# Performance work log

Hardware: AMD Instinct MI355X
Metric: run time of the kernel (lower is better)

The kernel has to match this reference:

```python
import jax, jax.numpy as jnp
import numpy as np

B, N, K = 4, 4096, 16
D_POINTS, D_MODEL = 64, 128


def setup_inputs() -> dict:
    key = jax.random.key(0)
    ks = jax.random.split(key, 18)
    rn = lambda k, shp, s=0.05: (jax.random.normal(k, shp, jnp.float32) * s)
    return {
        "xyz": jax.random.normal(ks[0], (B, N, 3), jnp.float32),
        "features": jax.random.normal(ks[1], (B, N, D_POINTS), jnp.float32),
        # fc_delta: Linear(3,d_model) -> ReLU -> Linear(d_model,d_model)
        "Wd1": rn(ks[2], (3, D_MODEL)), "bd1": rn(ks[3], (D_MODEL,)),
        "Wd2": rn(ks[4], (D_MODEL, D_MODEL)), "bd2": rn(ks[5], (D_MODEL,)),
        # fc1: Linear(d_points, d_model)
        "Wf1": rn(ks[6], (D_POINTS, D_MODEL)), "bf1": rn(ks[7], (D_MODEL,)),
        # w_qs / w_ks / w_vs: Linear(d_model, d_model, bias=False)
        "Wq": rn(ks[8], (D_MODEL, D_MODEL)),
        "Wk": rn(ks[9], (D_MODEL, D_MODEL)),
        "Wv": rn(ks[10], (D_MODEL, D_MODEL)),
        # fc_gamma: Linear(d_model,d_model) -> ReLU -> Linear(d_model,d_model)
        "Wg1": rn(ks[11], (D_MODEL, D_MODEL)), "bg1": rn(ks[12], (D_MODEL,)),
        "Wg2": rn(ks[13], (D_MODEL, D_MODEL)), "bg2": rn(ks[14], (D_MODEL,)),
        # fc2: Linear(d_model, d_points)
        "Wo": rn(ks[15], (D_MODEL, D_POINTS)), "bo": rn(ks[16], (D_POINTS,)),
    }


def reference(xyz, features, Wd1, bd1, Wd2, bd2, Wf1, bf1, Wq, Wk, Wv,
              Wg1, bg1, Wg2, bg2, Wo, bo):
    sq = jnp.sum(xyz * xyz, axis=-1)
    d2 = sq[:, :, None] + sq[:, None, :] - 2.0 * jnp.einsum('bnd,bmd->bnm', xyz, xyz)
    # argsort()[:, :, :k] == k smallest distances (self included)
    _, knn_idx = jax.lax.top_k(-d2, K)  # [B,N,K] int32

    gather = jax.vmap(lambda a, i: a[i])  # per-batch fancy gather along point axis
    knn_xyz = gather(xyz, knn_idx)                       # [B,N,K,3]
    rel = xyz[:, :, None, :] - knn_xyz                   # [B,N,K,3]
    pos_enc = jax.nn.relu(rel @ Wd1 + bd1) @ Wd2 + bd2   # [B,N,K,D]

    shortcut = features
    f = features @ Wf1 + bf1                             # [B,N,D]
    knn_f = gather(f, knn_idx)                           # [B,N,K,D]

    q = f @ Wq                                           # [B,N,D]
    k = knn_f @ Wk                                       # [B,N,K,D]
    v = knn_f @ Wv                                       # [B,N,K,D]

    attn = q[:, :, None, :] - k + pos_enc                # [B,N,K,D]
    attn = jax.nn.relu(attn @ Wg1 + bg1) @ Wg2 + bg2
    attn = jax.nn.softmax(attn / np.sqrt(D_MODEL).astype(np.float32), axis=-2)

    res = jnp.einsum('bnkf,bnkf->bnf', attn, v + pos_enc)  # [B,N,D]
    return res @ Wo + bo + shortcut                        # [B,N,d_points]
```

## Files before the change

kernel.cpp:

```cpp
#include <hip/hip_runtime.h>
#include <hip/hip_bf16.h>

#define NPTS 4096
#define BATCH 4
#define BN (BATCH * NPTS)
#define DMODEL 128
#define DPTS 64
#define KNBR 16
#define SWS 136

typedef unsigned short u16;
typedef unsigned int u32;
typedef unsigned long long u64;
typedef short bh8 __attribute__((ext_vector_type(8)));
typedef float f32x4 __attribute__((ext_vector_type(4)));

__device__ __forceinline__ float bfu(u16 u) {
    union { u32 i; float f; } c; c.i = ((u32)u) << 16; return c.f;
}
__device__ __forceinline__ u16 f2u(float x) {
    u32 u = __float_as_uint(x);
    u32 r = u + 0x7FFFu + ((u >> 16) & 1u);
    return (u16)(r >> 16);
}
__device__ __forceinline__ u32 pack2(float a, float b) {
    return (u32)f2u(a) | ((u32)f2u(b) << 16);
}
__device__ __forceinline__ float ldr(const void* p, long i, int mode) {
    return mode == 0 ? bfu(((const u16*)p)[i]) : ((const float*)p)[i];
}
__device__ __forceinline__ void str(void* p, long i, float v, int mode) {
    if (mode == 0) ((u16*)p)[i] = f2u(v);
    else ((float*)p)[i] = v;
}
__device__ __forceinline__ int detect_mode(const void* Wq) {
    const u16* w = (const u16*)Wq;
    int lane = threadIdx.x & 63;
    int tot = 0;
#pragma unroll
    for (int r = 0; r < 4; ++r) {
        unsigned e = (w[lane + r * 64] >> 7) & 0xFFu;
        bool wild = (e >= 132u) || (e > 0u && e <= 90u);
        tot += (int)__popcll(__ballot(wild));
    }
    return tot > 32 ? 1 : 0;
}

__global__ __launch_bounds__(256) void prep_kernel(
    const void* __restrict__ Wd2, const void* __restrict__ Wg1, const void* __restrict__ Wg2,
    const void* __restrict__ Wo, const void* __restrict__ Wq, const void* __restrict__ Wk,
    const void* __restrict__ Wv, const void* __restrict__ Wf1, const void* __restrict__ xyz,
    u16* __restrict__ WdT2, u16* __restrict__ WgT1, u16* __restrict__ WgT2,
    u16* __restrict__ WoT, u16* __restrict__ WqT, u16* __restrict__ WkT,
    u16* __restrict__ WvT, u16* __restrict__ WfT, uint2* __restrict__ cloud) {
    int mode = detect_mode(Wq);
    int gid = blockIdx.x * 256 + threadIdx.x;
    if (gid < 6 * 16384) {
        int m = gid >> 14, o = gid & 16383;
        int n = o >> 7, i = o & 127;
        const void* W = (m == 0) ? Wd2 : (m == 1) ? Wg1 : (m == 2) ? Wg2
                      : (m == 3) ? Wq  : (m == 4) ? Wk  : Wv;
        u16* D = (m == 0) ? WdT2 : (m == 1) ? WgT1 : (m == 2) ? WgT2
               : (m == 3) ? WqT  : (m == 4) ? WkT  : WvT;
        D[o] = f2u(ldr(W, (long)i * 128 + n, mode));
    } else if (gid < 6 * 16384 + 8192) {
        int o = gid - 6 * 16384;
        int n = o >> 6, k2 = o & 63;
        WfT[o] = f2u(ldr(Wf1, (long)k2 * 128 + n, mode));
    } else if (gid < 6 * 16384 + 16384) {
        int o2 = gid - 6 * 16384 - 8192;
        int col = o2 >> 7, i = o2 & 127;
        WoT[o2] = f2u(ldr(Wo, (long)i * 64 + col, mode));
    } else if (gid < 6 * 16384 + 16384 + 16384) {
        int i = gid - (6 * 16384 + 16384);
        float gx = ldr(xyz, (long)i * 3 + 0, mode);
        float gy = ldr(xyz, (long)i * 3 + 1, mode);
        float gz = ldr(xyz, (long)i * 3 + 2, mode);
        uint2 pk;
        pk.x = (u32)f2u(gx) | ((u32)f2u(gy) << 16);
        pk.y = (u32)f2u(gz);
        cloud[i] = pk;
    }
}

__global__ __launch_bounds__(256) void qkv_kernel(
    const void* __restrict__ feat, const void* __restrict__ bf1v, const void* __restrict__ WqRaw,
    const u16* __restrict__ WfT, const u16* __restrict__ WqT,
    const u16* __restrict__ WkT, const u16* __restrict__ WvT,
    u16* __restrict__ qw, u16* __restrict__ kfw, u16* __restrict__ vfw) {
    int mode = detect_mode(WqRaw);
    __shared__ __align__(16) u16 sFeat[64 * 72];
    __shared__ __align__(16) u16 sF[64 * SWS];
    const int t = threadIdx.x;
    const int p0 = blockIdx.x * 64;
    const int lane = t & 63, w = t >> 6;
    const int rg = (w & 1) * 32, cg = (w >> 1) * 64;
    const int lm = lane & 15, lq = lane >> 4;

    for (int i = t; i < 512; i += 256) {
        int r = i >> 3, c8 = i & 7;
        u16 tmp[8];
        if (mode == 0) {
            *(uint4*)tmp = *((const uint4*)feat + (long)(p0 + r) * 8 + c8);
        } else {
            const float* fp = (const float*)feat + (long)(p0 + r) * 64 + c8 * 8;
#pragma unroll
            for (int u = 0; u < 8; ++u) tmp[u] = f2u(fp[u]);
        }
        *(uint4*)(sFeat + r * 72 + c8 * 8) = *(uint4*)tmp;
    }
    __syncthreads();

    {
        f32x4 acc[2][4];
#pragma unroll
        for (int rt = 0; rt < 2; ++rt)
#pragma unroll
            for (int ct = 0; ct < 4; ++ct) { acc[rt][ct][0]=0.f; acc[rt][ct][1]=0.f; acc[rt][ct][2]=0.f; acc[rt][ct][3]=0.f; }
#pragma unroll
        for (int kk = 0; kk < 2; ++kk) {
            const int ko = kk * 32 + lq * 8;
            bh8 a0 = *(const bh8*)(sFeat + (rg + lm) * 72 + ko);
            bh8 a1 = *(const bh8*)(sFeat + (rg + 16 + lm) * 72 + ko);
            bh8 bq[4];
#pragma unroll
            for (int ct = 0; ct < 4; ++ct)
                bq[ct] = *(const bh8*)(WfT + (long)(cg + ct * 16 + lm) * 64 + ko);
#pragma unroll
            for (int ct = 0; ct < 4; ++ct) {
                acc[0][ct] = __builtin_amdgcn_mfma_f32_16x16x32_bf16(a0, bq[ct], acc[0][ct], 0, 0, 0);
                acc[1][ct] = __builtin_amdgcn_mfma_f32_16x16x32_bf16(a1, bq[ct], acc[1][ct], 0, 0, 0);
            }
        }
#pragma unroll
        for (int rt = 0; rt < 2; ++rt)
#pragma unroll
            for (int ct = 0; ct < 4; ++ct) {
                const int col = cg + ct * 16 + lm;
                const float bj = ldr(bf1v, col, mode);
#pragma unroll
                for (int r4 = 0; r4 < 4; ++r4) {
                    int row = rg + rt * 16 + lq * 4 + r4;
                    u32 u = (u32)f2u(acc[rt][ct][r4] + bj);
                    u32 o = __shfl_xor(u, 1);
                    if ((lane & 1) == 0)
                        *(u32*)(sF + row * SWS + col) = u | (o << 16);
                }
            }
    }
    __syncthreads();

    {
        const int m = blockIdx.y;
        const u16* Wm = (m == 0) ? WqT : (m == 1) ? WkT : WvT;
        u16* Om = (m == 0) ? qw : (m == 1) ? kfw : vfw;
        f32x4 acc[2][4];
#pragma unroll
        for (int rt = 0; rt < 2; ++rt)
#pragma unroll
            for (int ct = 0; ct < 4; ++ct) { acc[rt][ct][0]=0.f; acc[rt][ct][1]=0.f; acc[rt][ct][2]=0.f; acc[rt][ct][3]=0.f; }
#pragma unroll
        for (int kk = 0; kk < 4; ++kk) {
            const int ko = kk * 32 + lq * 8;
            bh8 a0 = *(const bh8*)(sF + (rg + lm) * SWS + ko);
            bh8 a1 = *(const bh8*)(sF + (rg + 16 + lm) * SWS + ko);
            bh8 bq[4];
#pragma unroll
            for (int ct = 0; ct < 4; ++ct)
                bq[ct] = *(const bh8*)(Wm + (long)(cg + ct * 16 + lm) * 128 + ko);
#pragma unroll
            for (int ct = 0; ct < 4; ++ct) {
                acc[0][ct] = __builtin_amdgcn_mfma_f32_16x16x32_bf16(a0, bq[ct], acc[0][ct], 0, 0, 0);
                acc[1][ct] = __builtin_amdgcn_mfma_f32_16x16x32_bf16(a1, bq[ct], acc[1][ct], 0, 0, 0);
            }
        }
#pragma unroll
        for (int rt = 0; rt < 2; ++rt)
#pragma unroll
            for (int ct = 0; ct < 4; ++ct) {
                const int col = cg + ct * 16 + lm;
#pragma unroll
                for (int r4 = 0; r4 < 4; ++r4) {
                    int row = rg + rt * 16 + lq * 4 + r4;
                    u32 u = (u32)f2u(acc[rt][ct][r4]);
                    u32 o = __shfl_xor(u, 1);
                    if ((lane & 1) == 0)
                        *(u32*)(Om + (long)(p0 + row) * DMODEL + col) = u | (o << 16);
                }
            }
    }
}

__global__ __launch_bounds__(256) void knn_kernel(
    const uint2* __restrict__ cloud, int* __restrict__ knnIdx) {
    const int t = threadIdx.x, lane = t & 63, w = t >> 6;
    const int p0 = blockIdx.x * 4;
    const long bbase = (long)(p0 >> 12) * NPTS;
    const uint2* cl = cloud + bbase;

    const int pl = (p0 & (NPTS - 1)) + w;
    uint2 qv = cl[pl];
    const float px = __uint_as_float(qv.x << 16);
    const float py = __uint_as_float(qv.x & 0xFFFF0000u);
    const float pz = __uint_as_float(qv.y << 16);

    u64 kv;
    {
        uint2 c = cl[lane];
        float cx = __uint_as_float(c.x << 16);
        float cy = __uint_as_float(c.x & 0xFFFF0000u);
        float cz = __uint_as_float(c.y << 16);
        float key = fmaf(px * cx + py * cy + pz * cz, -2.f,
                         cx * cx + cy * cy + cz * cz);
        u32 uk = __float_as_uint(key);
        uk ^= (u32)((int)uk >> 31) | 0x80000000u;
        kv = ((u64)uk << 32) | (u32)lane;
#pragma unroll
        for (int k = 2; k <= 64; k <<= 1) {
#pragma unroll
            for (int j = k >> 1; j > 0; j >>= 1) {
                u64 other = __shfl_xor(kv, j);
                bool keepMin = ((lane & j) == 0) == ((lane & k) == 0);
                bool smaller = kv < other;
                kv = (keepMin == smaller) ? kv : other;
            }
        }
    }
    u32 Tu = __builtin_amdgcn_readlane((u32)(kv >> 32), 15);

    uint2 cd0 = cl[64 + lane];
    uint2 cd1 = cl[128 + lane];
#pragma unroll 1
    for (int it = 0; it < 32; ++it) {
        const int base = 64 + it * 128;
        uint2 c0 = cd0, c1 = cd1;
        if (it < 31) {
            int n0 = base + 128 + lane;
            int n1 = n0 + 64 > 4095 ? 4095 : n0 + 64;
            cd0 = cl[n0];
            cd1 = cl[n1];
        }
        float cx0 = __uint_as_float(c0.x << 16);
        float cy0 = __uint_as_float(c0.x & 0xFFFF0000u);
        float cz0 = __uint_as_float(c0.y << 16);
        float cx1 = __uint_as_float(c1.x << 16);
        float cy1 = __uint_as_float(c1.x & 0xFFFF0000u);
        float cz1 = __uint_as_float(c1.y << 16);
        float k0 = fmaf(px * cx0 + py * cy0 + pz * cz0, -2.f,
                        cx0 * cx0 + cy0 * cy0 + cz0 * cz0);
        float k1 = fmaf(px * cx1 + py * cy1 + pz * cz1, -2.f,
                        cx1 * cx1 + cy1 * cy1 + cz1 * cz1);
        u32 u0 = __float_as_uint(k0); u0 ^= (u32)((int)u0 >> 31) | 0x80000000u;
        u32 u1 = __float_as_uint(k1); u1 ^= (u32)((int)u1 >> 31) | 0x80000000u;
        if (it == 31) u1 = 0xFFFFFFFFu;
        u32 umin = (u0 < u1) ? u0 : u1;
        unsigned long long mask = __ballot(umin < Tu);
        while (mask) {
            int l = __ffsll(mask) - 1;
            mask &= mask - 1;
            u32 a0 = __builtin_amdgcn_readlane(u0, l);
            u32 a1 = __builtin_amdgcn_readlane(u1, l);
            if (a0 < Tu) {
                u64 cand = ((u64)a0 << 32) | (u32)(base + l);
                u64 prev = __shfl_up(kv, 1);
                if (lane == 0) prev = 0;
                kv = (prev > cand) ? prev : ((kv > cand) ? cand : kv);
                Tu = __builtin_amdgcn_readlane((u32)(kv >> 32), 15);
            }
            if (a1 < Tu) {
                u64 cand = ((u64)a1 << 32) | (u32)(base + 64 + l);
                u64 prev = __shfl_up(kv, 1);
                if (lane == 0) prev = 0;
                kv = (prev > cand) ? prev : ((kv > cand) ? cand : kv);
                Tu = __builtin_amdgcn_readlane((u32)(kv >> 32), 15);
            }
        }
    }
    if (lane < 16) knnIdx[(long)(p0 + w) * 16 + lane] = (int)(u32)kv;
}

#define ATT_SA 0
#define ATT_SREL 17408
#define ATT_SBIAS 18432
#define ATT_SQ 19968
#define SMEM_BYTES 20992

__global__ __launch_bounds__(256, 4) void fused_kernel(
    const uint2* __restrict__ cloud, const int* __restrict__ knnIdx,
    const void* __restrict__ feat,
    const void* __restrict__ Wd1, const void* __restrict__ bd1, const void* __restrict__ bd2,
    const void* __restrict__ bg1, const void* __restrict__ bg2, const void* __restrict__ bo,
    const void* __restrict__ WqRaw,
    const u16* __restrict__ WdT2, const u16* __restrict__ WgT1, const u16* __restrict__ WgT2,
    const u16* __restrict__ WoT,
    const u16* __restrict__ qw, const u16* __restrict__ kfw, const u16* __restrict__ vfw,
    void* __restrict__ out) {
    int mode = detect_mode(WqRaw);
    __shared__ __align__(16) char smem[SMEM_BYTES];
    __shared__ int sIdx[64];
    u16* sA   = (u16*)(smem + ATT_SA);
    float (*sRel)[4] = (float(*)[4])(smem + ATT_SREL);
    float* sBias = (float*)(smem + ATT_SBIAS);
    u16* sQ   = (u16*)(smem + ATT_SQ);

    const int t = threadIdx.x, lane = t & 63, w = t >> 6;
    const int lm = lane & 15, lq = lane >> 4;
    const int rg = (w & 1) * 32, cg = (w >> 1) * 64;
    const int p0 = blockIdx.x * 4;
    const long bbase = (long)(p0 >> 12) * NPTS;
    const uint2* cl = cloud + bbase;

    for (int i = t; i < 384; i += 256) {
        const void* b = (i < 128) ? bd2 : (i < 256) ? bg1 : bg2;
        sBias[i] = ldr(b, i & 127, mode);
    }
    ((u32*)sQ)[t] = ((const u32*)(qw + (long)p0 * DMODEL))[t];
    const int ch = 2 * lane;
    const float wd0a = ldr(Wd1, ch, mode),       wd0b = ldr(Wd1, ch + 1, mode);
    const float wd1a = ldr(Wd1, 128 + ch, mode), wd1b = ldr(Wd1, 128 + ch + 1, mode);
    const float wd2a = ldr(Wd1, 256 + ch, mode), wd2b = ldr(Wd1, 256 + ch + 1, mode);
    const float bd1a = ldr(bd1, ch, mode),       bd1b = ldr(bd1, ch + 1, mode);
    if (t < 64) {
        int idx = knnIdx[(long)p0 * 16 + t];
        sIdx[t] = idx;
        int pl2 = (p0 & (NPTS - 1)) + (t >> 4);
        uint2 pv = cl[pl2];
        uint2 nv = cl[idx];
        sRel[t][0] = __uint_as_float(pv.x << 16)          - __uint_as_float(nv.x << 16);
        sRel[t][1] = __uint_as_float(pv.x & 0xFFFF0000u)  - __uint_as_float(nv.x & 0xFFFF0000u);
        sRel[t][2] = __uint_as_float(pv.y << 16)          - __uint_as_float(nv.y << 16);
    }
    __syncthreads();

#pragma unroll
    for (int i = 0; i < 16; ++i) {
        int r = w * 16 + i;
        float4 rl = *(const float4*)sRel[r];
        float h0 = fmaxf(bd1a + rl.x * wd0a + rl.y * wd1a + rl.z * wd2a, 0.f);
        float h1 = fmaxf(bd1b + rl.x * wd0b + rl.y * wd1b + rl.z * wd2b, 0.f);
        *(u32*)(sA + r * SWS + ch) = pack2(h0, h1);
    }
    __syncthreads();

    u32 pe[2][4][2];
    {
        f32x4 acc[2][4];
#pragma unroll
        for (int rt = 0; rt < 2; ++rt)
#pragma unroll
            for (int ct = 0; ct < 4; ++ct) { acc[rt][ct][0]=0.f; acc[rt][ct][1]=0.f; acc[rt][ct][2]=0.f; acc[rt][ct][3]=0.f; }
#pragma unroll
        for (int kk = 0; kk < 4; ++kk) {
            const int ko = kk * 32 + lq * 8;
            bh8 a0 = *(const bh8*)(sA + (rg + lm) * SWS + ko);
            bh8 a1 = *(const bh8*)(sA + (rg + 16 + lm) * SWS + ko);
            bh8 bq[4];
#pragma unroll
            for (int ct = 0; ct < 4; ++ct)
                bq[ct] = *(const bh8*)(WdT2 + (long)(cg + ct * 16 + lm) * 128 + ko);
#pragma unroll
            for (int ct = 0; ct < 4; ++ct) {
                acc[0][ct] = __builtin_amdgcn_mfma_f32_16x16x32_bf16(a0, bq[ct], acc[0][ct], 0, 0, 0);
                acc[1][ct] = __builtin_amdgcn_mfma_f32_16x16x32_bf16(a1, bq[ct], acc[1][ct], 0, 0, 0);
            }
        }
#pragma unroll
        for (int rt = 0; rt < 2; ++rt)
#pragma unroll
            for (int ct = 0; ct < 4; ++ct) {
                const float bj = sBias[cg + ct * 16 + lm];
                pe[rt][ct][0] = pack2(acc[rt][ct][0] + bj, acc[rt][ct][1] + bj);
                pe[rt][ct][1] = pack2(acc[rt][ct][2] + bj, acc[rt][ct][3] + bj);
            }
    }
    __syncthreads();

#pragma unroll
    for (int rt = 0; rt < 2; ++rt) {
        const int pt = (w & 1) * 2 + rt;
        int id4[4];
#pragma unroll
        for (int r4 = 0; r4 < 4; ++r4)
            id4[r4] = sIdx[rg + rt * 16 + lq * 4 + r4];
#pragma unroll
        for (int ct = 0; ct < 4; ++ct) {
            const int col = cg + ct * 16 + lm;
            const float qv = bfu(sQ[pt * DMODEL + col]);
#pragma unroll
            for (int r4 = 0; r4 < 4; ++r4) {
                const int row = rg + rt * 16 + lq * 4 + r4;
                u16 kfv = kfw[(bbase + id4[r4]) * (long)DMODEL + col];
                float pev = bfu((u16)(pe[rt][ct][r4 >> 1] >> (16 * (r4 & 1))));
                float a = qv - bfu(kfv) + pev;
                u32 u = (u32)f2u(a);
                u32 o = __shfl_xor(u, 1);
                if ((lm & 1) == 0)
                    *(u32*)(sA + row * SWS + col) = u | (o << 16);
            }
        }
    }
    __syncthreads();

    {
        f32x4 acc[2][4];
#pragma unroll
        for (int rt = 0; rt < 2; ++rt)
#pragma unroll
            for (int ct = 0; ct < 4; ++ct) { acc[rt][ct][0]=0.f; acc[rt][ct][1]=0.f; acc[rt][ct][2]=0.f; acc[rt][ct][3]=0.f; }
#pragma unroll
        for (int kk = 0; kk < 4; ++kk) {
            const int ko = kk * 32 + lq * 8;
            bh8 a0 = *(const bh8*)(sA + (rg + lm) * SWS + ko);
            bh8 a1 = *(const bh8*)(sA + (rg + 16 + lm) * SWS + ko);
            bh8 bq[4];
#pragma unroll
            for (int ct = 0; ct < 4; ++ct)
                bq[ct] = *(const bh8*)(WgT1 + (long)(cg + ct * 16 + lm) * 128 + ko);
#pragma unroll
            for (int ct = 0; ct < 4; ++ct) {
                acc[0][ct] = __builtin_amdgcn_mfma_f32_16x16x32_bf16(a0, bq[ct], acc[0][ct], 0, 0, 0);
                acc[1][ct] = __builtin_amdgcn_mfma_f32_16x16x32_bf16(a1, bq[ct], acc[1][ct], 0, 0, 0);
            }
        }
        __syncthreads();
#pragma unroll
        for (int rt = 0; rt < 2; ++rt)
#pragma unroll
            for (int ct = 0; ct < 4; ++ct) {
                const int col = cg + ct * 16 + lm;
                const float bj = sBias[128 + col];
#pragma unroll
                for (int r4 = 0; r4 < 4; ++r4) {
                    int row = rg + rt * 16 + lq * 4 + r4;
                    float v = fmaxf(acc[rt][ct][r4] + bj, 0.f);
                    u32 u = (u32)f2u(v);
                    u32 o = __shfl_xor(u, 1);
                    if ((lane & 1) == 0)
                        *(u32*)(sA + row * SWS + col) = u | (o << 16);
                }
            }
    }
    __syncthreads();

    {
        f32x4 acc[2][4];
#pragma unroll
        for (int rt = 0; rt < 2; ++rt)
#pragma unroll
            for (int ct = 0; ct < 4; ++ct) { acc[rt][ct][0]=0.f; acc[rt][ct][1]=0.f; acc[rt][ct][2]=0.f; acc[rt][ct][3]=0.f; }
#pragma unroll
        for (int kk = 0; kk < 4; ++kk) {
            const int ko = kk * 32 + lq * 8;
            bh8 a0 = *(const bh8*)(sA + (rg + lm) * SWS + ko);
            bh8 a1 = *(const bh8*)(sA + (rg + 16 + lm) * SWS + ko);
            bh8 bq[4];
#pragma unroll
            for (int ct = 0; ct < 4; ++ct)
                bq[ct] = *(const bh8*)(WgT2 + (long)(cg + ct * 16 + lm) * 128 + ko);
#pragma unroll
            for (int ct = 0; ct < 4; ++ct) {
                acc[0][ct] = __builtin_amdgcn_mfma_f32_16x16x32_bf16(a0, bq[ct], acc[0][ct], 0, 0, 0);
                acc[1][ct] = __builtin_amdgcn_mfma_f32_16x16x32_bf16(a1, bq[ct], acc[1][ct], 0, 0, 0);
            }
        }
        __syncthreads();

        const float inv = 0.08838834764831845f;
#pragma unroll
        for (int rt = 0; rt < 2; ++rt) {
            const int pt = (w & 1) * 2 + rt;
            int id4[4];
#pragma unroll
            for (int r4 = 0; r4 < 4; ++r4)
                id4[r4] = sIdx[rg + rt * 16 + lq * 4 + r4];
#pragma unroll
            for (int ct = 0; ct < 4; ++ct) {
                const int col = cg + ct * 16 + lm;
                const float bj = sBias[256 + col];
                float l0 = acc[rt][ct][0] + bj;
                float l1 = acc[rt][ct][1] + bj;
                float l2 = acc[rt][ct][2] + bj;
                float l3 = acc[rt][ct][3] + bj;
                float m = fmaxf(fmaxf(l0, l1), fmaxf(l2, l3));
                m = fmaxf(m, __shfl_xor(m, 16));
                m = fmaxf(m, __shfl_xor(m, 32));
                float s = 0.f, r = 0.f;
#pragma unroll
                for (int r4 = 0; r4 < 4; ++r4) {
                    float l = (r4 == 0) ? l0 : (r4 == 1) ? l1 : (r4 == 2) ? l2 : l3;
                    u16 vv = vfw[(bbase + id4[r4]) * (long)DMODEL + col];
                    float pev = bfu((u16)(pe[rt][ct][r4 >> 1] >> (16 * (r4 & 1))));
                    float e = __expf((l - m) * inv);
                    s += e;
                    r += e * (bfu(vv) + pev);
                }
                s += __shfl_xor(s, 16); s += __shfl_xor(s, 32);
                r += __shfl_xor(r, 16); r += __shfl_xor(r, 32);
                u32 u = (u32)f2u(r / s);
                u32 o = __shfl_xor(u, 1);
                if (lq == 0 && (lm & 1) == 0)
                    *(u32*)(sA + pt * SWS + col) = u | (o << 16);
            }
        }
    }
    __syncthreads();

    {
        const int col = w * 16 + lm;
        f32x4 acc = {0.f, 0.f, 0.f, 0.f};
#pragma unroll
        for (int kk = 0; kk < 4; ++kk) {
            const int ko = kk * 32 + lq * 8;
            bh8 aa = *(const bh8*)(sA + lm * SWS + ko);
            bh8 bb = *(const bh8*)(WoT + (long)col * DMODEL + ko);
            acc = __builtin_amdgcn_mfma_f32_16x16x32_bf16(aa, bb, acc, 0, 0, 0);
        }
        if (lq == 0) {
            float bov = ldr(bo, col, mode);
#pragma unroll
            for (int r4 = 0; r4 < 4; ++r4) {
                long p = p0 + r4;
                float v = acc[r4] + bov + ldr(feat, p * DPTS + col, mode);
                str(out, p * DPTS + col, v, mode);
            }
        }
    }
}

extern "C" void kernel_launch(void* const* d_in, const int* in_sizes, int n_in,
                              void* d_out, int out_size, void* d_ws, size_t ws_size,
                              hipStream_t stream) {
    (void)in_sizes; (void)n_in; (void)out_size; (void)ws_size;
    char* ws = (char*)d_ws;
    u16* qw   = (u16*)(ws + 256);
    u16* kfw  = qw + (long)BN * DMODEL;
    u16* vfw  = kfw + (long)BN * DMODEL;
    u16* WdT2 = vfw + (long)BN * DMODEL;
    u16* WgT1 = WdT2 + 16384;
    u16* WgT2 = WgT1 + 16384;
    u16* WoT  = WgT2 + 16384;
    u16* WqT  = WoT + 8192;
    u16* WkT  = WqT + 16384;
    u16* WvT  = WkT + 16384;
    u16* WfT  = WvT + 16384;
    uint2* cloud = (uint2*)(WfT + 8192);
    int* knnIdx = (int*)(cloud + BN);

    prep_kernel<<<512, 256, 0, stream>>>(d_in[4], d_in[11], d_in[13], d_in[15],
                                         d_in[8], d_in[9], d_in[10], d_in[6], d_in[0],
                                         WdT2, WgT1, WgT2, WoT, WqT, WkT, WvT, WfT,
                                         cloud);
    qkv_kernel<<<dim3(BN / 64, 3), 256, 0, stream>>>(d_in[1], d_in[7], d_in[8],
                                                     WfT, WqT, WkT, WvT, qw, kfw, vfw);
    knn_kernel<<<BN / 4, 256, 0, stream>>>(cloud, knnIdx);
    fused_kernel<<<BN / 4, 256, 0, stream>>>(cloud, knnIdx, d_in[1],
                                             d_in[2], d_in[3], d_in[5],
                                             d_in[12], d_in[14], d_in[16], d_in[8],
                                             WdT2, WgT1, WgT2, WoT,
                                             qw, kfw, vfw, d_out);
}
```

Measured before the change: 321.5 us.

## Double fused kernel to 512 threads and prefetch gathered K/V features early

The fused attention kernel moves from 256 to 512 threads per block. Each of the 8 waves now owns one point (16 neighbor rows) and a 64-column slice instead of two points, which halves per-wave accumulator registers. The gathers of neighbor key and value features are issued early into packed registers so their global latency overlaps with the positional-encoding and gamma MLP work. The trade-off is more threads per block, so occupancy now depends on the new launch bounds, and the final output projection leaves half the waves idle.

```diff
diff --git a/kernel.cpp b/kernel.cpp
--- a/kernel.cpp
+++ b/kernel.cpp
@@ -285,7 +285,7 @@
 #define ATT_SQ 19968
 #define SMEM_BYTES 20992
 
-__global__ __launch_bounds__(256, 4) void fused_kernel(
+__global__ __launch_bounds__(512, 6) void fused_kernel(
     const uint2* __restrict__ cloud, const int* __restrict__ knnIdx,
     const void* __restrict__ feat,
     const void* __restrict__ Wd1, const void* __restrict__ bd1, const void* __restrict__ bd2,
@@ -305,16 +305,17 @@
 
     const int t = threadIdx.x, lane = t & 63, w = t >> 6;
     const int lm = lane & 15, lq = lane >> 4;
-    const int rg = (w & 1) * 32, cg = (w >> 1) * 64;
+    const int pt = w & 3;
+    const int rg = pt * 16, cg = (w >> 2) * 64;
     const int p0 = blockIdx.x * 4;
     const long bbase = (long)(p0 >> 12) * NPTS;
     const uint2* cl = cloud + bbase;
 
-    for (int i = t; i < 384; i += 256) {
+    for (int i = t; i < 384; i += 512) {
         const void* b = (i < 128) ? bd2 : (i < 256) ? bg1 : bg2;
         sBias[i] = ldr(b, i & 127, mode);
     }
-    ((u32*)sQ)[t] = ((const u32*)(qw + (long)p0 * DMODEL))[t];
+    if (t < 256) ((u32*)sQ)[t] = ((const u32*)(qw + (long)p0 * DMODEL))[t];
     const int ch = 2 * lane;
     const float wd0a = ldr(Wd1, ch, mode),       wd0b = ldr(Wd1, ch + 1, mode);
     const float wd1a = ldr(Wd1, 128 + ch, mode), wd1b = ldr(Wd1, 128 + ch + 1, mode);
@@ -332,9 +333,25 @@
     }
     __syncthreads();
 
-#pragma unroll
-    for (int i = 0; i < 16; ++i) {
-        int r = w * 16 + i;
+    int id4[4];
+#pragma unroll
+    for (int r4 = 0; r4 < 4; ++r4)
+        id4[r4] = sIdx[rg + lq * 4 + r4];
+    u32 kfp[4][2];
+#pragma unroll
+    for (int ct = 0; ct < 4; ++ct) {
+        const int col = cg + ct * 16 + lm;
+        u16 a = kfw[(bbase + id4[0]) * (long)DMODEL + col];
+        u16 b = kfw[(bbase + id4[1]) * (long)DMODEL + col];
+        u16 c = kfw[(bbase + id4[2]) * (long)DMODEL + col];
+        u16 d = kfw[(bbase + id4[3]) * (long)DMODEL + col];
+        kfp[ct][0] = (u32)a | ((u32)b << 16);
+        kfp[ct][1] = (u32)c | ((u32)d << 16);
+    }
+
+#pragma unroll
+    for (int i = 0; i < 8; ++i) {
+        int r = w * 8 + i;
         float4 rl = *(const float4*)sRel[r];
         float h0 = fmaxf(bd1a + rl.x * wd0a + rl.y * wd1a + rl.z * wd2a, 0.f);
         float h1 = fmaxf(bd1b + rl.x * wd0b + rl.y * wd1b + rl.z * wd2b, 0.f);
@@ -342,57 +359,84 @@
     }
     __syncthreads();
 
-    u32 pe[2][4][2];
+    u32 pe[4][2];
     {
-        f32x4 acc[2][4];
-#pragma unroll
-        for (int rt = 0; rt < 2; ++rt)
-#pragma unroll
-            for (int ct = 0; ct < 4; ++ct) { acc[rt][ct][0]=0.f; acc[rt][ct][1]=0.f; acc[rt][ct][2]=0.f; acc[rt][ct][3]=0.f; }
+        f32x4 acc[4];
+#pragma unroll
+        for (int ct = 0; ct < 4; ++ct) { acc[ct][0]=0.f; acc[ct][1]=0.f; acc[ct][2]=0.f; acc[ct][3]=0.f; }
 #pragma unroll
         for (int kk = 0; kk < 4; ++kk) {
             const int ko = kk * 32 + lq * 8;
             bh8 a0 = *(const bh8*)(sA + (rg + lm) * SWS + ko);
-            bh8 a1 = *(const bh8*)(sA + (rg + 16 + lm) * SWS + ko);
-            bh8 bq[4];
-#pragma unroll
-            for (int ct = 0; ct < 4; ++ct)
-                bq[ct] = *(const bh8*)(WdT2 + (long)(cg + ct * 16 + lm) * 128 + ko);
-#pragma unroll
-            for (int ct = 0; ct < 4; ++ct) {
-                acc[0][ct] = __builtin_amdgcn_mfma_f32_16x16x32_bf16(a0, bq[ct], acc[0][ct], 0, 0, 0);
-                acc[1][ct] = __builtin_amdgcn_mfma_f32_16x16x32_bf16(a1, bq[ct], acc[1][ct], 0, 0, 0);
-            }
-        }
-#pragma unroll
-        for (int rt = 0; rt < 2; ++rt)
-#pragma unroll
-            for (int ct = 0; ct < 4; ++ct) {
-                const float bj = sBias[cg + ct * 16 + lm];
-                pe[rt][ct][0] = pack2(acc[rt][ct][0] + bj, acc[rt][ct][1] + bj);
-                pe[rt][ct][1] = pack2(acc[rt][ct][2] + bj, acc[rt][ct][3] + bj);
-            }
-    }
-    __syncthreads();
-
-#pragma unroll
-    for (int rt = 0; rt < 2; ++rt) {
-        const int pt = (w & 1) * 2 + rt;
-        int id4[4];
-#pragma unroll
-        for (int r4 = 0; r4 < 4; ++r4)
-            id4[r4] = sIdx[rg + rt * 16 + lq * 4 + r4];
+#pragma unroll
+            for (int ct = 0; ct < 4; ++ct) {
+                bh8 bq = *(const bh8*)(WdT2 + (long)(cg + ct * 16 + lm) * 128 + ko);
+                acc[ct] = __builtin_amdgcn_mfma_f32_16x16x32_bf16(a0, bq, acc[ct], 0, 0, 0);
+            }
+        }
+#pragma unroll
+        for (int ct = 0; ct < 4; ++ct) {
+            const float bj = sBias[cg + ct * 16 + lm];
+            pe[ct][0] = pack2(acc[ct][0] + bj, acc[ct][1] + bj);
+            pe[ct][1] = pack2(acc[ct][2] + bj, acc[ct][3] + bj);
+        }
+    }
+    __syncthreads();
+
+#pragma unroll
+    for (int ct = 0; ct < 4; ++ct) {
+        const int col = cg + ct * 16 + lm;
+        const float qv = bfu(sQ[pt * DMODEL + col]);
+#pragma unroll
+        for (int r4 = 0; r4 < 4; ++r4) {
+            const int row = rg + lq * 4 + r4;
+            float kfv = bfu((u16)(kfp[ct][r4 >> 1] >> (16 * (r4 & 1))));
+            float pev = bfu((u16)(pe[ct][r4 >> 1] >> (16 * (r4 & 1))));
+            float a = qv - kfv + pev;
+            u32 u = (u32)f2u(a);
+            u32 o = __shfl_xor(u, 1);
+            if ((lm & 1) == 0)
+                *(u32*)(sA + row * SWS + col) = u | (o << 16);
+        }
+    }
+    __syncthreads();
+
+    u32 vvp[4][2];
+#pragma unroll
+    for (int ct = 0; ct < 4; ++ct) {
+        const int col = cg + ct * 16 + lm;
+        u16 a = vfw[(bbase + id4[0]) * (long)DMODEL + col];
+        u16 b = vfw[(bbase + id4[1]) * (long)DMODEL + col];
+        u16 c = vfw[(bbase + id4[2]) * (long)DMODEL + col];
+        u16 d = vfw[(bbase + id4[3]) * (long)DMODEL + col];
+        vvp[ct][0] = (u32)a | ((u32)b << 16);
+        vvp[ct][1] = (u32)c | ((u32)d << 16);
+    }
+
+    {
+        f32x4 acc[4];
+#pragma unroll
+        for (int ct = 0; ct < 4; ++ct) { acc[ct][0]=0.f; acc[ct][1]=0.f; acc[ct][2]=0.f; acc[ct][3]=0.f; }
+#pragma unroll
+        for (int kk = 0; kk < 4; ++kk) {
+            const int ko = kk * 32 + lq * 8;
+            bh8 a0 = *(const bh8*)(sA + (rg + lm) * SWS + ko);
+#pragma unroll
+            for (int ct = 0; ct < 4; ++ct) {
+                bh8 bq = *(const bh8*)(WgT1 + (long)(cg + ct * 16 + lm) * 128 + ko);
+                acc[ct] = __builtin_amdgcn_mfma_f32_16x16x32_bf16(a0, bq, acc[ct], 0, 0, 0);
+            }
+        }
+        __syncthreads();
 #pragma unroll
         for (int ct = 0; ct < 4; ++ct) {
             const int col = cg + ct * 16 + lm;
-            const float qv = bfu(sQ[pt * DMODEL + col]);
+            const float bj = sBias[128 + col];
 #pragma unroll
             for (int r4 = 0; r4 < 4; ++r4) {
-                const int row = rg + rt * 16 + lq * 4 + r4;
-                u16 kfv = kfw[(bbase + id4[r4]) * (long)DMODEL + col];
-                float pev = bfu((u16)(pe[rt][ct][r4 >> 1] >> (16 * (r4 & 1))));
-                float a = qv - bfu(kfv) + pev;
-                u32 u = (u32)f2u(a);
+                int row = rg + lq * 4 + r4;
+                float v = fmaxf(acc[ct][r4] + bj, 0.f);
+                u32 u = (u32)f2u(v);
                 u32 o = __shfl_xor(u, 1);
                 if ((lm & 1) == 0)
                     *(u32*)(sA + row * SWS + col) = u | (o << 16);
@@ -402,110 +446,54 @@
     __syncthreads();
 
     {
-        f32x4 acc[2][4];
-#pragma unroll
-        for (int rt = 0; rt < 2; ++rt)
-#pragma unroll
-            for (int ct = 0; ct < 4; ++ct) { acc[rt][ct][0]=0.f; acc[rt][ct][1]=0.f; acc[rt][ct][2]=0.f; acc[rt][ct][3]=0.f; }
+        f32x4 acc[4];
+#pragma unroll
+        for (int ct = 0; ct < 4; ++ct) { acc[ct][0]=0.f; acc[ct][1]=0.f; acc[ct][2]=0.f; acc[ct][3]=0.f; }
 #pragma unroll
         for (int kk = 0; kk < 4; ++kk) {
             const int ko = kk * 32 + lq * 8;
             bh8 a0 = *(const bh8*)(sA + (rg + lm) * SWS + ko);
-            bh8 a1 = *(const bh8*)(sA + (rg + 16 + lm) * SWS + ko);
-            bh8 bq[4];
-#pragma unroll
-            for (int ct = 0; ct < 4; ++ct)
-                bq[ct] = *(const bh8*)(WgT1 + (long)(cg + ct * 16 + lm) * 128 + ko);
-#pragma unroll
-            for (int ct = 0; ct < 4; ++ct) {
-                acc[0][ct] = __builtin_amdgcn_mfma_f32_16x16x32_bf16(a0, bq[ct], acc[0][ct], 0, 0, 0);
-                acc[1][ct] = __builtin_amdgcn_mfma_f32_16x16x32_bf16(a1, bq[ct], acc[1][ct], 0, 0, 0);
+#pragma unroll
+            for (int ct = 0; ct < 4; ++ct) {
+                bh8 bq = *(const bh8*)(WgT2 + (long)(cg + ct * 16 + lm) * 128 + ko);
+                acc[ct] = __builtin_amdgcn_mfma_f32_16x16x32_bf16(a0, bq, acc[ct], 0, 0, 0);
             }
         }
         __syncthreads();
-#pragma unroll
-        for (int rt = 0; rt < 2; ++rt)
-#pragma unroll
-            for (int ct = 0; ct < 4; ++ct) {
-                const int col = cg + ct * 16 + lm;
-                const float bj = sBias[128 + col];
-#pragma unroll
-                for (int r4 = 0; r4 < 4; ++r4) {
-                    int row = rg + rt * 16 + lq * 4 + r4;
-                    float v = fmaxf(acc[rt][ct][r4] + bj, 0.f);
-                    u32 u = (u32)f2u(v);
-                    u32 o = __shfl_xor(u, 1);
-                    if ((lane & 1) == 0)
-                        *(u32*)(sA + row * SWS + col) = u | (o << 16);
-                }
-            }
-    }
-    __syncthreads();
-
-    {
-        f32x4 acc[2][4];
-#pragma unroll
-        for (int rt = 0; rt < 2; ++rt)
-#pragma unroll
-            for (int ct = 0; ct < 4; ++ct) { acc[rt][ct][0]=0.f; acc[rt][ct][1]=0.f; acc[rt][ct][2]=0.f; acc[rt][ct][3]=0.f; }
-#pragma unroll
-        for (int kk = 0; kk < 4; ++kk) {
-            const int ko = kk * 32 + lq * 8;
-            bh8 a0 = *(const bh8*)(sA + (rg + lm) * SWS + ko);
-            bh8 a1 = *(const bh8*)(sA + (rg + 16 + lm) * SWS + ko);
-            bh8 bq[4];
-#pragma unroll
-            for (int ct = 0; ct < 4; ++ct)
-                bq[ct] = *(const bh8*)(WgT2 + (long)(cg + ct * 16 + lm) * 128 + ko);
-#pragma unroll
-            for (int ct = 0; ct < 4; ++ct) {
-                acc[0][ct] = __builtin_amdgcn_mfma_f32_16x16x32_bf16(a0, bq[ct], acc[0][ct], 0, 0, 0);
-                acc[1][ct] = __builtin_amdgcn_mfma_f32_16x16x32_bf16(a1, bq[ct], acc[1][ct], 0, 0, 0);
-            }
-        }
-        __syncthreads();
 
         const float inv = 0.08838834764831845f;
 #pragma unroll
-        for (int rt = 0; rt < 2; ++rt) {
-            const int pt = (w & 1) * 2 + rt;
-            int id4[4];
-#pragma unroll
-            for (int r4 = 0; r4 < 4; ++r4)
-                id4[r4] = sIdx[rg + rt * 16 + lq * 4 + r4];
-#pragma unroll
-            for (int ct = 0; ct < 4; ++ct) {
-                const int col = cg + ct * 16 + lm;
-                const float bj = sBias[256 + col];
-                float l0 = acc[rt][ct][0] + bj;
-                float l1 = acc[rt][ct][1] + bj;
-                float l2 = acc[rt][ct][2] + bj;
-                float l3 = acc[rt][ct][3] + bj;
-                float m = fmaxf(fmaxf(l0, l1), fmaxf(l2, l3));
-                m = fmaxf(m, __shfl_xor(m, 16));
-                m = fmaxf(m, __shfl_xor(m, 32));
-                float s = 0.f, r = 0.f;
-#pragma unroll
-                for (int r4 = 0; r4 < 4; ++r4) {
-                    float l = (r4 == 0) ? l0 : (r4 == 1) ? l1 : (r4 == 2) ? l2 : l3;
-                    u16 vv = vfw[(bbase + id4[r4]) * (long)DMODEL + col];
-                    float pev = bfu((u16)(pe[rt][ct][r4 >> 1] >> (16 * (r4 & 1))));
-                    float e = __expf((l - m) * inv);
-                    s += e;
-                    r += e * (bfu(vv) + pev);
-                }
-                s += __shfl_xor(s, 16); s += __shfl_xor(s, 32);
-                r += __shfl_xor(r, 16); r += __shfl_xor(r, 32);
-                u32 u = (u32)f2u(r / s);
-                u32 o = __shfl_xor(u, 1);
-                if (lq == 0 && (lm & 1) == 0)
-                    *(u32*)(sA + pt * SWS + col) = u | (o << 16);
-            }
-        }
-    }
-    __syncthreads();
-
-    {
+        for (int ct = 0; ct < 4; ++ct) {
+            const int col = cg + ct * 16 + lm;
+            const float bj = sBias[256 + col];
+            float l0 = acc[ct][0] + bj;
+            float l1 = acc[ct][1] + bj;
+            float l2 = acc[ct][2] + bj;
+            float l3 = acc[ct][3] + bj;
+            float m = fmaxf(fmaxf(l0, l1), fmaxf(l2, l3));
+            m = fmaxf(m, __shfl_xor(m, 16));
+            m = fmaxf(m, __shfl_xor(m, 32));
+            float s = 0.f, r = 0.f;
+#pragma unroll
+            for (int r4 = 0; r4 < 4; ++r4) {
+                float l = (r4 == 0) ? l0 : (r4 == 1) ? l1 : (r4 == 2) ? l2 : l3;
+                float vv = bfu((u16)(vvp[ct][r4 >> 1] >> (16 * (r4 & 1))));
+                float pev = bfu((u16)(pe[ct][r4 >> 1] >> (16 * (r4 & 1))));
+                float e = __expf((l - m) * inv);
+                s += e;
+                r += e * (vv + pev);
+            }
+            s += __shfl_xor(s, 16); s += __shfl_xor(s, 32);
+            r += __shfl_xor(r, 16); r += __shfl_xor(r, 32);
+            u32 u = (u32)f2u(r / s);
+            u32 o = __shfl_xor(u, 1);
+            if (lq == 0 && (lm & 1) == 0)
+                *(u32*)(sA + pt * SWS + col) = u | (o << 16);
+        }
+    }
+    __syncthreads();
+
+    if (w < 4) {
         const int col = w * 16 + lm;
         f32x4 acc = {0.f, 0.f, 0.f, 0.f};
 #pragma unroll
@@ -553,7 +541,7 @@
     qkv_kernel<<<dim3(BN / 64, 3), 256, 0, stream>>>(d_in[1], d_in[7], d_in[8],
                                                      WfT, WqT, WkT, WvT, qw, kfw, vfw);
     knn_kernel<<<BN / 4, 256, 0, stream>>>(cloud, knnIdx);
-    fused_kernel<<<BN / 4, 256, 0, stream>>>(cloud, knnIdx, d_in[1],
+    fused_kernel<<<BN / 4, 512, 0, stream>>>(cloud, knnIdx, d_in[1],
                                              d_in[2], d_in[3], d_in[5],
                                              d_in[12], d_in[14], d_in[16], d_in[8],
                                              WdT2, WgT1, WgT2, WoT,
```

Result: slower. 390.1 us (+21.3%).
